# Kernel optimization log

Hardware: AMD Instinct MI355X
Metric: run time of the kernel (lower is better)

## Reference

```python
import jax, jax.numpy as jnp
import numpy as np

N = 1024
DIM = 3
H = 64  # hidden width from sizes=[64, 64]


def _mlp(inp, W1, b1, W2, b2, W3, b3):
    # hk.nets.MLP(sizes + [1], activation=softplus): activate all but last layer
    h = jax.nn.softplus(inp @ W1 + b1)
    h = jax.nn.softplus(h @ W2 + b2)
    return h @ W3 + b3


def setup_inputs() -> dict:
    key = jax.random.key(0)
    ks = jax.random.split(key, 14)
    x = jax.random.normal(ks[0], (N, DIM), dtype=jnp.float32)
    t = jax.random.uniform(ks[1], (), dtype=jnp.float32)
    s = 0.01  # TruncatedNormal(0.01) init
    return {
        "x": x,
        "t": t,
        "xi_W1": jax.random.normal(ks[2], (2, H), jnp.float32) * s,
        "xi_b1": jnp.zeros((H,), jnp.float32),
        "xi_W2": jax.random.normal(ks[3], (H, H), jnp.float32) * s,
        "xi_b2": jnp.zeros((H,), jnp.float32),
        "xi_W3": jax.random.normal(ks[4], (H, 1), jnp.float32) * s,
        "xi_b3": jnp.zeros((1,), jnp.float32),
        "eta_W1": jax.random.normal(ks[5], (2, H), jnp.float32) * s,
        "eta_b1": jnp.zeros((H,), jnp.float32),
        "eta_W2": jax.random.normal(ks[6], (H, H), jnp.float32) * s,
        "eta_b2": jnp.zeros((H,), jnp.float32),
        "eta_W3": jax.random.normal(ks[7], (H, 1), jnp.float32) * s,
        "eta_b3": jnp.zeros((1,), jnp.float32),
    }


def reference(x, t, xi_W1, xi_b1, xi_W2, xi_b2, xi_W3, xi_b3,
              eta_W1, eta_b1, eta_W2, eta_b2, eta_W3, eta_b3):
    n = x.shape[0]
    # one-body term: xi(|x_i|, t) * x_i
    r = jnp.linalg.norm(x, axis=-1)  # (n,)
    inp_xi = jnp.stack([r, jnp.full_like(r, t)], axis=-1)  # (n, 2)
    res = _mlp(inp_xi, xi_W1, xi_b1, xi_W2, xi_b2, xi_W3, xi_b3) * x  # (n, dim)
    # two-body term: sum_j eta(|x_i - x_j|, t) * (x_i - x_j)
    rij = x[:, None, :] - x[None, :, :]  # (n, n, dim)
    eye = jnp.eye(n, dtype=x.dtype)
    rdist = jnp.linalg.norm(rij + eye[..., None], axis=-1) * (1.0 - eye)  # (n, n)
    inp_eta = jnp.stack([rdist, jnp.full_like(rdist, t)], axis=-1)  # (n, n, 2)
    eta_out = _mlp(inp_eta, eta_W1, eta_b1, eta_W2, eta_b2, eta_W3, eta_b3)  # (n, n, 1)
    res = res + (eta_out * rij).sum(axis=1)
    return res
```

## Files before the change

kernel.cpp:

```cpp
#include <hip/hip_runtime.h>
#include <math.h>


#define TABLE_N 2048
#define RMAX 16.0f
#define NPART 1024
#define EB 129
#define XB 64
#define DELTA (RMAX / (float)TABLE_N)

__device__ __forceinline__ float sp_fast(float v) {
    return __logf(1.f + __expf(v));
}

__global__ __launch_bounds__(256) void k1_table_onebody(
    const float* __restrict__ x, const float* __restrict__ t_ptr,
    const float* __restrict__ xiW1, const float* __restrict__ xib1,
    const float* __restrict__ xiW2, const float* __restrict__ xib2,
    const float* __restrict__ xiW3, const float* __restrict__ xib3,
    const float* __restrict__ eW1,  const float* __restrict__ eb1,
    const float* __restrict__ eW2,  const float* __restrict__ eb2,
    const float* __restrict__ eW3,  const float* __restrict__ eb3,
    float* __restrict__ out, float* __restrict__ table)
{
    __shared__ __align__(16) float w2s[4096];
    __shared__ __align__(16) float w1s[128];
    __shared__ __align__(16) float b1s[64];
    __shared__ __align__(16) float b2s[64];
    __shared__ __align__(16) float w3s[64];
    __shared__ __align__(16) float hbuf[4][128];

    const int tid = threadIdx.x;
    const int b   = blockIdx.x;
    const bool tb = (b < EB);

    const float* __restrict__ W1 = tb ? eW1 : xiW1;
    const float* __restrict__ B1 = tb ? eb1 : xib1;
    const float* __restrict__ W2 = tb ? eW2 : xiW2;
    const float* __restrict__ B2 = tb ? eb2 : xib2;
    const float* __restrict__ W3 = tb ? eW3 : xiW3;

    {
        const float4* src = (const float4*)W2;
        float4* dst = (float4*)w2s;
        #pragma unroll
        for (int i2 = 0; i2 < 4; ++i2) dst[tid + 256 * i2] = src[tid + 256 * i2];
        if (tid < 128)      w1s[tid]       = W1[tid];
        else if (tid < 192) b1s[tid - 128] = B1[tid - 128];
        else                b2s[tid - 192] = B2[tid - 192];
        if (tid < 64)       w3s[tid]       = W3[tid];
    }

    const float t  = t_ptr[0];
    const float B3 = tb ? eb3[0] : xib3[0];
    const int lane = tid & 63;
    const int w    = tid >> 6;
    const int base = tb ? (16 * b + 4 * w) : (16 * (b - EB) + 4 * w);

    __syncthreads();

    #pragma unroll
    for (int p = 0; p < 2; ++p) {
        const int e0 = base + 2 * p, e1 = e0 + 1;
        float r0, r1;
        float x0x = 0.f, x0y = 0.f, x0z = 0.f, x1x = 0.f, x1y = 0.f, x1z = 0.f;
        if (tb) {
            r0 = (float)e0 * DELTA;
            r1 = (float)e1 * DELTA;
        } else {
            x0x = x[3 * e0]; x0y = x[3 * e0 + 1]; x0z = x[3 * e0 + 2];
            x1x = x[3 * e1]; x1y = x[3 * e1 + 1]; x1z = x[3 * e1 + 2];
            r0 = sqrtf(fmaf(x0x, x0x, fmaf(x0y, x0y, x0z * x0z)));
            r1 = sqrtf(fmaf(x1x, x1x, fmaf(x1y, x1y, x1z * x1z)));
        }
        const float w1a = w1s[lane], w1b = w1s[64 + lane], b1v = b1s[lane];
        hbuf[w][lane]      = sp_fast(fmaf(r0, w1a, fmaf(t, w1b, b1v)));
        hbuf[w][64 + lane] = sp_fast(fmaf(r1, w1a, fmaf(t, w1b, b1v)));
        float z0 = b2s[lane], z1 = z0;
        #pragma unroll
        for (int k = 0; k < 64; k += 4) {
            float4 ha = *(const float4*)&hbuf[w][k];
            float4 hb = *(const float4*)&hbuf[w][64 + k];
            float wa = w2s[k * 64 + lane];
            float wbv = w2s[(k + 1) * 64 + lane];
            float wc = w2s[(k + 2) * 64 + lane];
            float wd = w2s[(k + 3) * 64 + lane];
            z0 = fmaf(ha.x, wa,  z0); z1 = fmaf(hb.x, wa,  z1);
            z0 = fmaf(ha.y, wbv, z0); z1 = fmaf(hb.y, wbv, z1);
            z0 = fmaf(ha.z, wc,  z0); z1 = fmaf(hb.z, wc,  z1);
            z0 = fmaf(ha.w, wd,  z0); z1 = fmaf(hb.w, wd,  z1);
        }
        float q0 = sp_fast(z0) * w3s[lane];
        float q1 = sp_fast(z1) * w3s[lane];
        #pragma unroll
        for (int off = 32; off > 0; off >>= 1) {
            q0 += __shfl_xor(q0, off);
            q1 += __shfl_xor(q1, off);
        }
        if (lane == 0) {
            if (tb) {
                if (e0 <= TABLE_N) table[e0] = q0 + B3;
                if (e1 <= TABLE_N) table[e1] = q1 + B3;
            } else {
                float f0 = q0 + B3, f1 = q1 + B3;
                out[3 * e0] = f0 * x0x; out[3 * e0 + 1] = f0 * x0y; out[3 * e0 + 2] = f0 * x0z;
                out[3 * e1] = f1 * x1x; out[3 * e1 + 1] = f1 * x1y; out[3 * e1 + 2] = f1 * x1z;
            }
        }
    }
}

__global__ __launch_bounds__(256) void k2_twobody(
    const float* __restrict__ x, const float* __restrict__ table,
    float* __restrict__ out)
{
    __shared__ float xs[NPART], ys[NPART], zs[NPART];
    __shared__ __align__(16) float tab[2052];
    const int tid = threadIdx.x;

    for (int idx = tid; idx < 3 * NPART; idx += 256) {
        float v = x[idx];
        int j = idx / 3, c = idx - 3 * j;
        if (c == 0) xs[j] = v;
        else if (c == 1) ys[j] = v;
        else zs[j] = v;
    }
    {
        const float4* src = (const float4*)table;
        float4* dst = (float4*)tab;
        for (int i2 = tid; i2 < 513; i2 += 256) dst[i2] = src[i2];
    }
    __syncthreads();

    const int wave = tid >> 6, lane = tid & 63;
    const int i = blockIdx.x * 4 + wave;
    const float xi = xs[i], yi = ys[i], zi = zs[i];
    float ax = 0.f, ay = 0.f, az = 0.f;
    const float scale = (float)TABLE_N / RMAX;
    #pragma unroll
    for (int it = 0; it < NPART / 64; ++it) {
        int j = it * 64 + lane;
        float dx = xi - xs[j], dy = yi - ys[j], dz = zi - zs[j];
        float r = sqrtf(fmaf(dx, dx, fmaf(dy, dy, dz * dz)));
        float u = fminf(r * scale, (float)TABLE_N - 0.001f);
        int i0 = (int)u;
        float fr = u - (float)i0;
        float t0 = tab[i0], t1 = tab[i0 + 1];
        float f = fmaf(fr, t1 - t0, t0);
        ax = fmaf(f, dx, ax);
        ay = fmaf(f, dy, ay);
        az = fmaf(f, dz, az);
    }
    #pragma unroll
    for (int off = 32; off > 0; off >>= 1) {
        ax += __shfl_xor(ax, off);
        ay += __shfl_xor(ay, off);
        az += __shfl_xor(az, off);
    }
    if (lane == 0) {
        out[3 * i]     += ax;
        out[3 * i + 1] += ay;
        out[3 * i + 2] += az;
    }
}

extern "C" void kernel_launch(void* const* d_in, const int* in_sizes, int n_in,
                              void* d_out, int out_size, void* d_ws, size_t ws_size,
                              hipStream_t stream) {
    const float* x     = (const float*)d_in[0];
    const float* t     = (const float*)d_in[1];
    const float* xiW1  = (const float*)d_in[2];
    const float* xib1  = (const float*)d_in[3];
    const float* xiW2  = (const float*)d_in[4];
    const float* xib2  = (const float*)d_in[5];
    const float* xiW3  = (const float*)d_in[6];
    const float* xib3  = (const float*)d_in[7];
    const float* eW1   = (const float*)d_in[8];
    const float* eb1   = (const float*)d_in[9];
    const float* eW2   = (const float*)d_in[10];
    const float* eb2   = (const float*)d_in[11];
    const float* eW3   = (const float*)d_in[12];
    const float* eb3   = (const float*)d_in[13];
    float* out   = (float*)d_out;
    float* table = (float*)d_ws;

    k1_table_onebody<<<EB + XB, 256, 0, stream>>>(
        x, t, xiW1, xib1, xiW2, xib2, xiW3, xib3,
        eW1, eb1, eW2, eb2, eW3, eb3, out, table);
    k2_twobody<<<256, 256, 0, stream>>>(x, table, out);
}
```

Measured before the change: 91.25 us.

## Shrink eta lookup table, spread MLP work over more blocks, fuse one-body output into k2

Reduces the eta lookup table from 2048 to 512 entries and halves per-block work in the first kernel, so it launches 193 blocks with one pass each instead of two. The one-body term is now written to workspace and combined in the two-body kernel, which writes the output directly instead of doing a read-modify-write. The two-body kernel also loads x with float4 copies in AoS form rather than splitting it into SoA with divisions. The coarser table loosens interpolation accuracy, and the AoS layout gives stride-3 shared-memory reads in the inner loop.

Measured after the change: 85.44 us. 1.07x faster.

```diff
diff --git a/kernel.cpp b/kernel.cpp
--- a/kernel.cpp
+++ b/kernel.cpp
@@ -2,12 +2,13 @@
 #include <math.h>
 
 
-#define TABLE_N 2048
+#define TABLE_N 512
 #define RMAX 16.0f
 #define NPART 1024
-#define EB 129
-#define XB 64
+#define EBLK 65
+#define XBLK 128
 #define DELTA (RMAX / (float)TABLE_N)
+#define FV_OFF 516
 
 __device__ __forceinline__ float sp_fast(float v) {
     return __logf(1.f + __expf(v));
@@ -21,7 +22,7 @@
     const float* __restrict__ eW1,  const float* __restrict__ eb1,
     const float* __restrict__ eW2,  const float* __restrict__ eb2,
     const float* __restrict__ eW3,  const float* __restrict__ eb3,
-    float* __restrict__ out, float* __restrict__ table)
+    float* __restrict__ ws)
 {
     __shared__ __align__(16) float w2s[4096];
     __shared__ __align__(16) float w1s[128];
@@ -30,9 +31,12 @@
     __shared__ __align__(16) float w3s[64];
     __shared__ __align__(16) float hbuf[4][128];
 
+    float* __restrict__ table = ws;
+    float* __restrict__ fvals = ws + FV_OFF;
+
     const int tid = threadIdx.x;
     const int b   = blockIdx.x;
-    const bool tb = (b < EB);
+    const bool tb = (b < EBLK);
 
     const float* __restrict__ W1 = tb ? eW1 : xiW1;
     const float* __restrict__ B1 = tb ? eb1 : xib1;
@@ -55,92 +59,84 @@
     const float B3 = tb ? eb3[0] : xib3[0];
     const int lane = tid & 63;
     const int w    = tid >> 6;
-    const int base = tb ? (16 * b + 4 * w) : (16 * (b - EB) + 4 * w);
+    const int e0   = (tb ? 8 * b : 8 * (b - EBLK)) + 2 * w;
+    const int e1   = e0 + 1;
 
+    float r0, r1;
+    if (tb) {
+        r0 = (float)e0 * DELTA;
+        r1 = (float)e1 * DELTA;
+    } else {
+        float ax_ = x[3 * e0], ay_ = x[3 * e0 + 1], az_ = x[3 * e0 + 2];
+        float bx_ = x[3 * e1], by_ = x[3 * e1 + 1], bz_ = x[3 * e1 + 2];
+        r0 = sqrtf(fmaf(ax_, ax_, fmaf(ay_, ay_, az_ * az_)));
+        r1 = sqrtf(fmaf(bx_, bx_, fmaf(by_, by_, bz_ * bz_)));
+    }
     __syncthreads();
 
+    const float w1a = w1s[lane], w1b = w1s[64 + lane], b1v = b1s[lane];
+    hbuf[w][lane]      = sp_fast(fmaf(r0, w1a, fmaf(t, w1b, b1v)));
+    hbuf[w][64 + lane] = sp_fast(fmaf(r1, w1a, fmaf(t, w1b, b1v)));
+    float z0 = b2s[lane], z1 = z0;
     #pragma unroll
-    for (int p = 0; p < 2; ++p) {
-        const int e0 = base + 2 * p, e1 = e0 + 1;
-        float r0, r1;
-        float x0x = 0.f, x0y = 0.f, x0z = 0.f, x1x = 0.f, x1y = 0.f, x1z = 0.f;
+    for (int k = 0; k < 64; k += 4) {
+        float4 ha = *(const float4*)&hbuf[w][k];
+        float4 hb = *(const float4*)&hbuf[w][64 + k];
+        float wa  = w2s[k * 64 + lane];
+        float wbv = w2s[(k + 1) * 64 + lane];
+        float wc  = w2s[(k + 2) * 64 + lane];
+        float wd  = w2s[(k + 3) * 64 + lane];
+        z0 = fmaf(ha.x, wa,  z0); z1 = fmaf(hb.x, wa,  z1);
+        z0 = fmaf(ha.y, wbv, z0); z1 = fmaf(hb.y, wbv, z1);
+        z0 = fmaf(ha.z, wc,  z0); z1 = fmaf(hb.z, wc,  z1);
+        z0 = fmaf(ha.w, wd,  z0); z1 = fmaf(hb.w, wd,  z1);
+    }
+    float q0 = sp_fast(z0) * w3s[lane];
+    float q1 = sp_fast(z1) * w3s[lane];
+    #pragma unroll
+    for (int off = 32; off > 0; off >>= 1) {
+        q0 += __shfl_xor(q0, off);
+        q1 += __shfl_xor(q1, off);
+    }
+    if (lane == 0) {
         if (tb) {
-            r0 = (float)e0 * DELTA;
-            r1 = (float)e1 * DELTA;
+            if (e0 <= TABLE_N) table[e0] = q0 + B3;
+            if (e1 <= TABLE_N) table[e1] = q1 + B3;
         } else {
-            x0x = x[3 * e0]; x0y = x[3 * e0 + 1]; x0z = x[3 * e0 + 2];
-            x1x = x[3 * e1]; x1y = x[3 * e1 + 1]; x1z = x[3 * e1 + 2];
-            r0 = sqrtf(fmaf(x0x, x0x, fmaf(x0y, x0y, x0z * x0z)));
-            r1 = sqrtf(fmaf(x1x, x1x, fmaf(x1y, x1y, x1z * x1z)));
-        }
-        const float w1a = w1s[lane], w1b = w1s[64 + lane], b1v = b1s[lane];
-        hbuf[w][lane]      = sp_fast(fmaf(r0, w1a, fmaf(t, w1b, b1v)));
-        hbuf[w][64 + lane] = sp_fast(fmaf(r1, w1a, fmaf(t, w1b, b1v)));
-        float z0 = b2s[lane], z1 = z0;
-        #pragma unroll
-        for (int k = 0; k < 64; k += 4) {
-            float4 ha = *(const float4*)&hbuf[w][k];
-            float4 hb = *(const float4*)&hbuf[w][64 + k];
-            float wa = w2s[k * 64 + lane];
-            float wbv = w2s[(k + 1) * 64 + lane];
-            float wc = w2s[(k + 2) * 64 + lane];
-            float wd = w2s[(k + 3) * 64 + lane];
-            z0 = fmaf(ha.x, wa,  z0); z1 = fmaf(hb.x, wa,  z1);
-            z0 = fmaf(ha.y, wbv, z0); z1 = fmaf(hb.y, wbv, z1);
-            z0 = fmaf(ha.z, wc,  z0); z1 = fmaf(hb.z, wc,  z1);
-            z0 = fmaf(ha.w, wd,  z0); z1 = fmaf(hb.w, wd,  z1);
-        }
-        float q0 = sp_fast(z0) * w3s[lane];
-        float q1 = sp_fast(z1) * w3s[lane];
-        #pragma unroll
-        for (int off = 32; off > 0; off >>= 1) {
-            q0 += __shfl_xor(q0, off);
-            q1 += __shfl_xor(q1, off);
-        }
-        if (lane == 0) {
-            if (tb) {
-                if (e0 <= TABLE_N) table[e0] = q0 + B3;
-                if (e1 <= TABLE_N) table[e1] = q1 + B3;
-            } else {
-                float f0 = q0 + B3, f1 = q1 + B3;
-                out[3 * e0] = f0 * x0x; out[3 * e0 + 1] = f0 * x0y; out[3 * e0 + 2] = f0 * x0z;
-                out[3 * e1] = f1 * x1x; out[3 * e1 + 1] = f1 * x1y; out[3 * e1 + 2] = f1 * x1z;
-            }
+            fvals[e0] = q0 + B3;
+            fvals[e1] = q1 + B3;
         }
     }
 }
 
 __global__ __launch_bounds__(256) void k2_twobody(
-    const float* __restrict__ x, const float* __restrict__ table,
+    const float* __restrict__ x, const float* __restrict__ ws,
     float* __restrict__ out)
 {
-    __shared__ float xs[NPART], ys[NPART], zs[NPART];
-    __shared__ __align__(16) float tab[2052];
+    __shared__ __align__(16) float xsoa[3 * NPART];
+    __shared__ __align__(16) float tab[516];
     const int tid = threadIdx.x;
 
-    for (int idx = tid; idx < 3 * NPART; idx += 256) {
-        float v = x[idx];
-        int j = idx / 3, c = idx - 3 * j;
-        if (c == 0) xs[j] = v;
-        else if (c == 1) ys[j] = v;
-        else zs[j] = v;
-    }
     {
-        const float4* src = (const float4*)table;
-        float4* dst = (float4*)tab;
-        for (int i2 = tid; i2 < 513; i2 += 256) dst[i2] = src[i2];
+        const float4* src = (const float4*)x;
+        float4* dst = (float4*)xsoa;
+        #pragma unroll
+        for (int i2 = 0; i2 < 3; ++i2) dst[tid + 256 * i2] = src[tid + 256 * i2];
+        const float4* ts = (const float4*)ws;
+        float4* td = (float4*)tab;
+        if (tid < 129) td[tid] = ts[tid];
     }
     __syncthreads();
 
     const int wave = tid >> 6, lane = tid & 63;
     const int i = blockIdx.x * 4 + wave;
-    const float xi = xs[i], yi = ys[i], zi = zs[i];
+    const float xi = xsoa[3 * i], yi = xsoa[3 * i + 1], zi = xsoa[3 * i + 2];
     float ax = 0.f, ay = 0.f, az = 0.f;
     const float scale = (float)TABLE_N / RMAX;
     #pragma unroll
     for (int it = 0; it < NPART / 64; ++it) {
         int j = it * 64 + lane;
-        float dx = xi - xs[j], dy = yi - ys[j], dz = zi - zs[j];
+        float dx = xi - xsoa[3 * j], dy = yi - xsoa[3 * j + 1], dz = zi - xsoa[3 * j + 2];
         float r = sqrtf(fmaf(dx, dx, fmaf(dy, dy, dz * dz)));
         float u = fminf(r * scale, (float)TABLE_N - 0.001f);
         int i0 = (int)u;
@@ -158,9 +154,10 @@
         az += __shfl_xor(az, off);
     }
     if (lane == 0) {
-        out[3 * i]     += ax;
-        out[3 * i + 1] += ay;
-        out[3 * i + 2] += az;
+        float fi = ws[FV_OFF + i];
+        out[3 * i]     = fmaf(fi, xi, ax);
+        out[3 * i + 1] = fmaf(fi, yi, ay);
+        out[3 * i + 2] = fmaf(fi, zi, az);
     }
 }
 
@@ -181,11 +178,11 @@
     const float* eb2   = (const float*)d_in[11];
     const float* eW3   = (const float*)d_in[12];
     const float* eb3   = (const float*)d_in[13];
-    float* out   = (float*)d_out;
-    float* table = (float*)d_ws;
+    float* out = (float*)d_out;
+    float* ws  = (float*)d_ws;
 
-    k1_table_onebody<<<EB + XB, 256, 0, stream>>>(
+    k1_table_onebody<<<EBLK + XBLK, 256, 0, stream>>>(
         x, t, xiW1, xib1, xiW2, xib2, xiW3, xib3,
-        eW1, eb1, eW2, eb2, eW3, eb3, out, table);
-    k2_twobody<<<256, 256, 0, stream>>>(x, table, out);
+        eW1, eb1, eW2, eb2, eW3, eb3, ws);
+    k2_twobody<<<256, 256, 0, stream>>>(x, ws, out);
 }
```
